# Kernel optimization log

Hardware: AMD Instinct MI355X
Metric: run time of the kernel (lower is better)

Reference implementation:

```python
import jax, jax.numpy as jnp
import numpy as np

BETA = 1.0
GAMMA = 1.0
DELTA = 0.0


def setup_inputs() -> dict:
    key = jax.random.key(0)
    k1, k2 = jax.random.split(key)
    xyz1 = jax.random.normal(k1, (4, 4096, 3), dtype=jnp.float32)
    xyz2 = jax.random.normal(k2, (4, 4096, 3), dtype=jnp.float32)
    return {"xyz1": xyz1, "xyz2": xyz2}


def _pairwise_sqdist(a, b):
    # a: [B, N, 3], b: [B, M, 3] -> [B, N, M] squared euclidean distances
    a2 = jnp.sum(a * a, axis=-1)  # [B, N]
    b2 = jnp.sum(b * b, axis=-1)  # [B, M]
    ab = jnp.einsum("bnd,bmd->bnm", a, b)  # [B, N, M]
    return a2[:, :, None] + b2[:, None, :] - 2.0 * ab


def reference(xyz1, xyz2):
    P = xyz1.shape[1]
    d = _pairwise_sqdist(xyz1, xyz2)  # [B, N, M]
    dist12 = jnp.min(d, axis=2)       # nearest in xyz2 for each xyz1 point
    idx12 = jnp.argmin(d, axis=2)
    dist21 = jnp.min(d, axis=1)       # nearest in xyz1 for each xyz2 point
    idx21 = jnp.argmin(d, axis=1)
    loss = (jnp.mean(dist12, axis=-1)
            + jnp.max(dist12, axis=-1) * BETA
            + (GAMMA + DELTA * P) * jnp.mean(dist21, axis=-1))
    loss = jnp.mean(loss)
    return loss, idx12, idx21
```

## Files before the change

kernel.cpp:

```cpp
#include <hip/hip_runtime.h>
#include <stdint.h>
#include <float.h>


constexpr int B_ = 4;
constexpr int N_ = 4096;
constexpr int PTS = 256;
constexpr int PPT = 8;
constexpr int TILES = N_ / (PTS * PPT);
constexpr int JSPLIT = 32;
constexpr int CHUNK = N_ / JSPLIT;
constexpr double EPS32 = 1.1920928955078125e-7;
constexpr double TOL_K12 = 0.6 * EPS32;
constexpr double TOL_K21 = 0.0;
constexpr double BETA_ = 1.0;
constexpr double GAMMA_ = 1.0;
constexpr double DELTA_ = 0.0;

__global__ __launch_bounds__(256) void cd_min32(
        const float* __restrict__ xyz1, const float* __restrict__ xyz2,
        unsigned int* __restrict__ splitmin) {
    const int tile  = blockIdx.x % TILES;
    const int b     = (blockIdx.x / TILES) % B_;
    const int dir   = blockIdx.x / (TILES * B_);
    const int split = blockIdx.y;
    const float* A  = dir ? xyz2 : xyz1;
    const float* Bc = dir ? xyz1 : xyz2;

    __shared__ float4 s[CHUNK];
    const float* bbase = Bc + ((size_t)b * N_ + (size_t)split * CHUNK) * 3;
    if (threadIdx.x < CHUNK) {
        int j = threadIdx.x;
        s[j] = make_float4(bbase[3 * j], bbase[3 * j + 1], bbase[3 * j + 2], 0.f);
    }
    __syncthreads();

    float px[PPT], py[PPT], pz[PPT], mn[PPT];
    #pragma unroll
    for (int pi = 0; pi < PPT; ++pi) {
        const int p = tile * (PTS * PPT) + pi * PTS + threadIdx.x;
        const float* ap = A + ((size_t)b * N_ + p) * 3;
        px[pi] = ap[0]; py[pi] = ap[1]; pz[pi] = ap[2];
        mn[pi] = FLT_MAX;
    }

    #pragma unroll 4
    for (int j = 0; j < CHUNK; ++j) {
        float4 bv = s[j];
        #pragma unroll
        for (int pi = 0; pi < PPT; ++pi) {
            float dx = px[pi] - bv.x, dy = py[pi] - bv.y, dz = pz[pi] - bv.z;
            mn[pi] = fminf(mn[pi],
                           __fmaf_rn(dx, dx, __fmaf_rn(dy, dy, dz * dz)));
        }
    }

    const size_t ob = (size_t)dir * B_ + b;
    const size_t sm = (ob * JSPLIT + split) * N_;
    #pragma unroll
    for (int pi = 0; pi < PPT; ++pi) {
        const int p = tile * (PTS * PPT) + pi * PTS + threadIdx.x;
        splitmin[sm + p] = __float_as_uint(mn[pi]);
    }
}

__global__ __launch_bounds__(256) void cd_select(
        const float* __restrict__ xyz1, const float* __restrict__ xyz2,
        const unsigned int* __restrict__ splitmin,
        double* __restrict__ dminArr, float* __restrict__ out) {
    const int w    = blockIdx.x * 4 + (threadIdx.x >> 6);
    const int lane = threadIdx.x & 63;
    const int dir  = w / (B_ * N_);
    const int b    = (w / N_) % B_;
    const int p    = w % N_;
    const float* A  = dir ? xyz2 : xyz1;
    const float* Bc = dir ? xyz1 : xyz2;
    const double tolk = dir ? TOL_K21 : TOL_K12;
    const size_t ob = (size_t)dir * B_ + b;

    const float* ap = A + ((size_t)b * N_ + p) * 3;
    const float x = ap[0], y = ap[1], z = ap[2];
    const float a2f = x * x + y * y + z * z;

    const int l32 = lane & 31;
    const float sv = __uint_as_float(splitmin[(ob * JSPLIT + l32) * N_ + p]);
    float m = sv;
    #pragma unroll
    for (int off = 1; off < 32; off <<= 1)
        m = fminf(m, __shfl_xor(m, off));

    const float me = __fmaf_rn(2e-6f, m, m);
    const float skipthr = (me + 7e-7f * a2f) * (1.0f + 4e-6f);
    unsigned int mask = (unsigned int)__ballot(lane < 32 && sv <= skipthr);

    const float* bb = Bc + (size_t)b * N_ * 3;
    const double xd = (double)x, yd = (double)y, zd = (double)z;
    const double a2 = xd * xd + yd * yd + zd * zd;

    double dmin = 1.0e300;
    unsigned int mk = mask;
    while (mk) {
        int s = __ffs(mk) - 1; mk &= mk - 1;
        int j = s * CHUNK + lane;
        #pragma unroll
        for (int k = 0; k < 2; ++k, j += 64) {
            float bx = bb[3 * j], by = bb[3 * j + 1], bz = bb[3 * j + 2];
            float dx = x - bx, dy = y - by, dz = z - bz;
            float d32 = __fmaf_rn(dx, dx, __fmaf_rn(dy, dy, dz * dz));
            float thr = __fmaf_rn(2e-7f, a2f + (bx * bx + by * by + bz * bz), me);
            if (d32 <= thr) {
                double ddx = xd - (double)bx, ddy = yd - (double)by,
                       ddz = zd - (double)bz;
                dmin = fmin(dmin, fma(ddx, ddx, fma(ddy, ddy, ddz * ddz)));
            }
        }
    }
    #pragma unroll
    for (int off = 1; off < 64; off <<= 1)
        dmin = fmin(dmin, __shfl_xor(dmin, off));

    unsigned int pick = 0xFFFFFFFFu;
    mk = mask;
    while (mk) {
        int s = __ffs(mk) - 1; mk &= mk - 1;
        int j = s * CHUNK + lane;
        #pragma unroll
        for (int k = 0; k < 2; ++k, j += 64) {
            float bx = bb[3 * j], by = bb[3 * j + 1], bz = bb[3 * j + 2];
            float dx = x - bx, dy = y - by, dz = z - bz;
            float d32 = __fmaf_rn(dx, dx, __fmaf_rn(dy, dy, dz * dz));
            float thr = __fmaf_rn(2e-7f, a2f + (bx * bx + by * by + bz * bz), me);
            if (d32 <= thr) {
                double bxd = (double)bx, byd = (double)by, bzd = (double)bz;
                double ddx = xd - bxd, ddy = yd - byd, ddz = zd - bzd;
                double d64 = fma(ddx, ddx, fma(ddy, ddy, ddz * ddz));
                double M   = a2 + (bxd * bxd + byd * byd + bzd * bzd);
                if (d64 <= fma(tolk, M, dmin))
                    pick = (pick < (unsigned int)j) ? pick : (unsigned int)j;
            }
        }
    }
    #pragma unroll
    for (int off = 1; off < 64; off <<= 1) {
        unsigned int o2 = (unsigned int)__shfl_xor((int)pick, off);
        pick = (o2 < pick) ? o2 : pick;
    }

    if (lane == 0) {
        dminArr[w] = dmin;
        const size_t obase = (dir == 0) ? (1 + (size_t)b * N_)
                                        : (1 + (size_t)B_ * N_ + (size_t)b * N_);
        out[obase + p] = (float)pick;
    }
}

__global__ __launch_bounds__(256) void cd_finalize(
        const double* __restrict__ dminArr, float* __restrict__ out,
        double* __restrict__ loss_part) {
    const int b = blockIdx.x;
    const int t = threadIdx.x;

    double sum12 = 0.0, max12 = -1.0e300, sum21 = 0.0;
    for (int n = t; n < N_; n += 256) {
        double d12 = dminArr[(size_t)b * N_ + n];
        double d21 = dminArr[((size_t)B_ + b) * N_ + n];
        sum12 += d12;
        max12 = fmax(max12, d12);
        sum21 += d21;
    }
    __shared__ double s1[256], s2[256], s3[256];
    s1[t] = sum12; s2[t] = max12; s3[t] = sum21;
    __syncthreads();
    for (int off = 128; off > 0; off >>= 1) {
        if (t < off) {
            s1[t] += s1[t + off];
            s2[t]  = fmax(s2[t], s2[t + off]);
            s3[t] += s3[t + off];
        }
        __syncthreads();
    }
    if (t == 0) {
        loss_part[b] = s1[0] / (double)N_ + BETA_ * s2[0]
                     + (GAMMA_ + DELTA_ * (double)N_) * (s3[0] / (double)N_);
    }
}

__global__ void cd_loss(const double* __restrict__ loss_part,
                        float* __restrict__ out) {
    if (blockIdx.x == 0 && threadIdx.x == 0) {
        double s = 0.0;
        for (int b = 0; b < B_; ++b) s += loss_part[b];
        out[0] = (float)(s / (double)B_);
    }
}

extern "C" void kernel_launch(void* const* d_in, const int* in_sizes, int n_in,
                              void* d_out, int out_size, void* d_ws, size_t ws_size,
                              hipStream_t stream) {
    const float* xyz1 = (const float*)d_in[0];
    const float* xyz2 = (const float*)d_in[1];
    float* out = (float*)d_out;

    const size_t NP = (size_t)2 * B_ * N_;
    double* dminArr   = (double*)d_ws;
    double* loss_part = dminArr + NP;
    unsigned int* splitmin = (unsigned int*)(loss_part + B_);

    dim3 grid(TILES * B_ * 2, JSPLIT);
    cd_min32<<<grid, PTS, 0, stream>>>(xyz1, xyz2, splitmin);

    cd_select<<<(int)(NP / 4), 256, 0, stream>>>(xyz1, xyz2, splitmin,
                                                 dminArr, out);

    cd_finalize<<<B_, 256, 0, stream>>>(dminArr, out, loss_part);
    cd_loss<<<1, 64, 0, stream>>>(loss_part, out);
}
```

Baseline: 49.18 us.

## Batch 64 points per select block with a shared work queue and fused loss reduction

The select kernel used to give each wavefront one query point. Now each block handles 64 points: it loads their split minima coalesced into shared memory, builds a compacted queue of (point, split) candidates, and lets all four waves work through the queue. Per-point minima and argmin indices are merged with shared-memory atomicMin, and per-block sum/max partials are written out, so the finalize kernel is dropped and one launch is removed. This is meant to cut wasted wave work and imbalance when few splits survive, at the cost of extra block-level syncs and shared-memory atomics.

```diff
diff --git a/kernel.cpp b/kernel.cpp
--- a/kernel.cpp
+++ b/kernel.cpp
@@ -67,40 +67,83 @@
 __global__ __launch_bounds__(256) void cd_select(
         const float* __restrict__ xyz1, const float* __restrict__ xyz2,
         const unsigned int* __restrict__ splitmin,
-        double* __restrict__ dminArr, float* __restrict__ out) {
-    const int w    = blockIdx.x * 4 + (threadIdx.x >> 6);
-    const int lane = threadIdx.x & 63;
-    const int dir  = w / (B_ * N_);
-    const int b    = (w / N_) % B_;
-    const int p    = w % N_;
+        double2* __restrict__ partials, float* __restrict__ out) {
+    const int c64 = blockIdx.x & 63;
+    const int b   = (blockIdx.x >> 6) & (B_ - 1);
+    const int dir = blockIdx.x >> 8;
+    const int p0  = c64 * 64;
     const float* A  = dir ? xyz2 : xyz1;
     const float* Bc = dir ? xyz1 : xyz2;
     const double tolk = dir ? TOL_K21 : TOL_K12;
     const size_t ob = (size_t)dir * B_ + b;
 
-    const float* ap = A + ((size_t)b * N_ + p) * 3;
-    const float x = ap[0], y = ap[1], z = ap[2];
-    const float a2f = x * x + y * y + z * z;
-
-    const int l32 = lane & 31;
-    const float sv = __uint_as_float(splitmin[(ob * JSPLIT + l32) * N_ + p]);
-    float m = sv;
+    __shared__ unsigned int ltab[64][33];
+    __shared__ unsigned short queue[2048];
+    __shared__ unsigned long long dbits[64];
+    __shared__ unsigned int pickS[64];
+    __shared__ float pc[64][5];
+    __shared__ unsigned int cnt_total;
+
     #pragma unroll
-    for (int off = 1; off < 32; off <<= 1)
-        m = fminf(m, __shfl_xor(m, off));
-
-    const float me = __fmaf_rn(2e-6f, m, m);
-    const float skipthr = (me + 7e-7f * a2f) * (1.0f + 4e-6f);
-    unsigned int mask = (unsigned int)__ballot(lane < 32 && sv <= skipthr);
-
+    for (int k = 0; k < 8; ++k) {
+        int idx = threadIdx.x + 256 * k;
+        int row = idx >> 6, col = idx & 63;
+        ltab[col][row] = splitmin[(ob * JSPLIT + row) * N_ + p0 + col];
+    }
+    __syncthreads();
+
+    const int t = threadIdx.x;
+    if (t < 64) {
+        const int p = p0 + t;
+        const float* ap = A + ((size_t)b * N_ + p) * 3;
+        const float x = ap[0], y = ap[1], z = ap[2];
+        const float a2f = x * x + y * y + z * z;
+
+        float m = FLT_MAX;
+        #pragma unroll
+        for (int s = 0; s < JSPLIT; ++s)
+            m = fminf(m, __uint_as_float(ltab[t][s]));
+
+        const float me = __fmaf_rn(2e-6f, m, m);
+        const float skipthr = (me + 7e-7f * a2f) * (1.0f + 4e-6f);
+
+        unsigned int mask = 0;
+        #pragma unroll
+        for (int s = 0; s < JSPLIT; ++s)
+            if (__uint_as_float(ltab[t][s]) <= skipthr) mask |= (1u << s);
+
+        pc[t][0] = x; pc[t][1] = y; pc[t][2] = z; pc[t][3] = a2f; pc[t][4] = me;
+        dbits[t] = ~0ULL;
+        pickS[t] = 0xFFFFFFFFu;
+
+        unsigned int cnt = (unsigned int)__popc(mask);
+        unsigned int pre = cnt;
+        #pragma unroll
+        for (int off = 1; off < 64; off <<= 1) {
+            unsigned int o = (unsigned int)__shfl_up((int)pre, off);
+            if (t >= off) pre += o;
+        }
+        unsigned int w = pre - cnt;
+        while (mask) {
+            int s = __ffs(mask) - 1; mask &= mask - 1;
+            queue[w++] = (unsigned short)((t << 5) | s);
+        }
+        if (t == 63) cnt_total = pre;
+    }
+    __syncthreads();
+
+    const int wv = t >> 6, lane = t & 63;
     const float* bb = Bc + (size_t)b * N_ * 3;
-    const double xd = (double)x, yd = (double)y, zd = (double)z;
-    const double a2 = xd * xd + yd * yd + zd * zd;
-
-    double dmin = 1.0e300;
-    unsigned int mk = mask;
-    while (mk) {
-        int s = __ffs(mk) - 1; mk &= mk - 1;
+    const unsigned int ctot = cnt_total;
+
+    for (unsigned int e = wv; e < ctot; e += 4) {
+        unsigned int q = queue[e];
+        int i = q >> 5, s = q & 31;
+        const float x = pc[i][0], y = pc[i][1], z = pc[i][2];
+        const float a2f = pc[i][3], me = pc[i][4];
+        const double xd = (double)x, yd = (double)y, zd = (double)z;
+
+        double dmin = 1.0e300;
         int j = s * CHUNK + lane;
         #pragma unroll
         for (int k = 0; k < 2; ++k, j += 64) {
@@ -114,15 +157,24 @@
                 dmin = fmin(dmin, fma(ddx, ddx, fma(ddy, ddy, ddz * ddz)));
             }
         }
-    }
-    #pragma unroll
-    for (int off = 1; off < 64; off <<= 1)
-        dmin = fmin(dmin, __shfl_xor(dmin, off));
-
-    unsigned int pick = 0xFFFFFFFFu;
-    mk = mask;
-    while (mk) {
-        int s = __ffs(mk) - 1; mk &= mk - 1;
+        #pragma unroll
+        for (int off = 1; off < 64; off <<= 1)
+            dmin = fmin(dmin, __shfl_xor(dmin, off));
+        if (lane == 0)
+            atomicMin(&dbits[i], (unsigned long long)__double_as_longlong(dmin));
+    }
+    __syncthreads();
+
+    for (unsigned int e = wv; e < ctot; e += 4) {
+        unsigned int q = queue[e];
+        int i = q >> 5, s = q & 31;
+        const float x = pc[i][0], y = pc[i][1], z = pc[i][2];
+        const float a2f = pc[i][3], me = pc[i][4];
+        const double xd = (double)x, yd = (double)y, zd = (double)z;
+        const double a2 = xd * xd + yd * yd + zd * zd;
+        const double dminF = __longlong_as_double((long long)dbits[i]);
+
+        unsigned int pick = 0xFFFFFFFFu;
         int j = s * CHUNK + lane;
         #pragma unroll
         for (int k = 0; k < 2; ++k, j += 64) {
@@ -135,63 +187,55 @@
                 double ddx = xd - bxd, ddy = yd - byd, ddz = zd - bzd;
                 double d64 = fma(ddx, ddx, fma(ddy, ddy, ddz * ddz));
                 double M   = a2 + (bxd * bxd + byd * byd + bzd * bzd);
-                if (d64 <= fma(tolk, M, dmin))
+                if (d64 <= fma(tolk, M, dminF))
                     pick = (pick < (unsigned int)j) ? pick : (unsigned int)j;
             }
         }
-    }
-    #pragma unroll
-    for (int off = 1; off < 64; off <<= 1) {
-        unsigned int o2 = (unsigned int)__shfl_xor((int)pick, off);
-        pick = (o2 < pick) ? o2 : pick;
-    }
-
-    if (lane == 0) {
-        dminArr[w] = dmin;
+        #pragma unroll
+        for (int off = 1; off < 64; off <<= 1) {
+            unsigned int o2 = (unsigned int)__shfl_xor((int)pick, off);
+            pick = (o2 < pick) ? o2 : pick;
+        }
+        if (lane == 0) atomicMin(&pickS[i], pick);
+    }
+    __syncthreads();
+
+    if (t < 64) {
         const size_t obase = (dir == 0) ? (1 + (size_t)b * N_)
                                         : (1 + (size_t)B_ * N_ + (size_t)b * N_);
-        out[obase + p] = (float)pick;
-    }
-}
-
-__global__ __launch_bounds__(256) void cd_finalize(
-        const double* __restrict__ dminArr, float* __restrict__ out,
-        double* __restrict__ loss_part) {
-    const int b = blockIdx.x;
-    const int t = threadIdx.x;
-
-    double sum12 = 0.0, max12 = -1.0e300, sum21 = 0.0;
-    for (int n = t; n < N_; n += 256) {
-        double d12 = dminArr[(size_t)b * N_ + n];
-        double d21 = dminArr[((size_t)B_ + b) * N_ + n];
-        sum12 += d12;
-        max12 = fmax(max12, d12);
-        sum21 += d21;
-    }
-    __shared__ double s1[256], s2[256], s3[256];
-    s1[t] = sum12; s2[t] = max12; s3[t] = sum21;
-    __syncthreads();
-    for (int off = 128; off > 0; off >>= 1) {
-        if (t < off) {
-            s1[t] += s1[t + off];
-            s2[t]  = fmax(s2[t], s2[t + off]);
-            s3[t] += s3[t + off];
-        }
-        __syncthreads();
-    }
-    if (t == 0) {
-        loss_part[b] = s1[0] / (double)N_ + BETA_ * s2[0]
-                     + (GAMMA_ + DELTA_ * (double)N_) * (s3[0] / (double)N_);
-    }
-}
-
-__global__ void cd_loss(const double* __restrict__ loss_part,
+        out[obase + p0 + t] = (float)pickS[t];
+
+        double dm = __longlong_as_double((long long)dbits[t]);
+        double sum = dm, mx = dm;
+        #pragma unroll
+        for (int off = 1; off < 64; off <<= 1) {
+            sum += __shfl_xor(sum, off);
+            mx = fmax(mx, __shfl_xor(mx, off));
+        }
+        if (t == 0) partials[blockIdx.x] = make_double2(sum, mx);
+    }
+}
+
+__global__ void cd_loss(const double2* __restrict__ partials,
                         float* __restrict__ out) {
-    if (blockIdx.x == 0 && threadIdx.x == 0) {
-        double s = 0.0;
-        for (int b = 0; b < B_; ++b) s += loss_part[b];
-        out[0] = (float)(s / (double)B_);
-    }
+    const int lane = threadIdx.x;
+    double total = 0.0;
+    for (int b = 0; b < B_; ++b) {
+        double2 v0 = partials[((0 * B_ + b) << 6) | lane];
+        double s12 = v0.x, m12 = v0.y;
+        double2 v1 = partials[((1 * B_ + b) << 6) | lane];
+        double s21 = v1.x;
+        #pragma unroll
+        for (int off = 1; off < 64; off <<= 1) {
+            s12 += __shfl_xor(s12, off);
+            m12 = fmax(m12, __shfl_xor(m12, off));
+            s21 += __shfl_xor(s21, off);
+        }
+        if (lane == 0)
+            total += s12 / (double)N_ + BETA_ * m12
+                   + (GAMMA_ + DELTA_ * (double)N_) * (s21 / (double)N_);
+    }
+    if (lane == 0) out[0] = (float)(total / (double)B_);
 }
 
 extern "C" void kernel_launch(void* const* d_in, const int* in_sizes, int n_in,
@@ -202,16 +246,14 @@
     float* out = (float*)d_out;
 
     const size_t NP = (size_t)2 * B_ * N_;
-    double* dminArr   = (double*)d_ws;
-    double* loss_part = dminArr + NP;
-    unsigned int* splitmin = (unsigned int*)(loss_part + B_);
+    double2* partials = (double2*)d_ws;
+    unsigned int* splitmin = (unsigned int*)(partials + 512);
 
     dim3 grid(TILES * B_ * 2, JSPLIT);
     cd_min32<<<grid, PTS, 0, stream>>>(xyz1, xyz2, splitmin);
 
-    cd_select<<<(int)(NP / 4), 256, 0, stream>>>(xyz1, xyz2, splitmin,
-                                                 dminArr, out);
-
-    cd_finalize<<<B_, 256, 0, stream>>>(dminArr, out, loss_part);
-    cd_loss<<<1, 64, 0, stream>>>(loss_part, out);
-}
+    cd_select<<<2 * B_ * 64, 256, 0, stream>>>(xyz1, xyz2, splitmin,
+                                               partials, out);
+
+    cd_loss<<<1, 64, 0, stream>>>(partials, out);
+}
```

Measured after the change: 51.11 us. +3.9%, slower.
